# Performance work log

Measured on AMD Instinct MI355X. Metric: run time of the kernel, lower is better.

The kernel has to match this reference:

```python
import jax, jax.numpy as jnp
import numpy as np

H = 4        # nhead
TEMP = 0.1   # temperature
TOP_K = 5
SHAPE_EPS = 1e-5


def _ln(x, g, b):
    m = x.mean(-1, keepdims=True)
    v = ((x - m) ** 2).mean(-1, keepdims=True)
    return (x - m) / jnp.sqrt(v + SHAPE_EPS) * g + b


def _mha(x, Wqkv, bqkv, Wo, bo):
    B, L, D = x.shape
    Dh = D // H
    qkv = x @ Wqkv.T + bqkv                     # [B,L,3D]
    q, k, v = jnp.split(qkv, 3, axis=-1)
    q = q.reshape(B, L, H, Dh)
    k = k.reshape(B, L, H, Dh)
    v = v.reshape(B, L, H, Dh)
    att = jnp.einsum('bqhd,bkhd->bhqk', q, k) * (1.0 / np.sqrt(Dh))
    att = jax.nn.softmax(att, axis=-1)
    o = jnp.einsum('bhqk,bkhd->bqhd', att, v).reshape(B, L, D)
    return o @ Wo.T + bo


def _pattern_encoder(x, cls_token, Wqkv, bqkv, Wo, bo, ln1_g, ln1_b,
                     W1, b1, W2, b2, ln2_g, ln2_b, proj_W, proj_b, proj_g, proj_bb):
    B, L, D = x.shape
    h = jnp.concatenate([jnp.broadcast_to(cls_token, (B, 1, D)), x], axis=1)  # [B,L+1,D]
    for i in range(Wqkv.shape[0]):  # num_layers=2, post-norm (PyTorch default)
        a = _mha(h, Wqkv[i], bqkv[i], Wo[i], bo[i])
        h = _ln(h + a, ln1_g[i], ln1_b[i])
        f = jax.nn.gelu(h @ W1[i].T + b1[i], approximate=False) @ W2[i].T + b2[i]
        h = _ln(h + f, ln2_g[i], ln2_b[i])
    cls_out = h[:, 0, :]
    return _ln(cls_out @ proj_W.T + proj_b, proj_g, proj_bb)  # [B,d_repr]


def _value_encoder(xm, vW1, vb1, v_g, v_b, vW2, vb2):
    hh = _ln(xm @ vW1.T + vb1, v_g, v_b)
    return jax.nn.gelu(hh, approximate=False) @ vW2.T + vb2


def setup_inputs() -> dict:
    B, L, D, DR, N, P, NL = 64, 512, 512, 128, 10000, 96, 2
    key = jax.random.key(0)
    ks = jax.random.split(key, 16)
    sc = 0.02
    inp = {
        'query': jax.random.normal(ks[0], (B, L, D), jnp.float32),
        'memory_keys': jax.random.normal(ks[1], (N, DR), jnp.float32),
        'memory_values': jax.random.normal(ks[2], (N, P, D), jnp.float32),
        'cls_token': jax.random.normal(ks[3], (1, 1, D), jnp.float32) * sc,
        'Wqkv': jax.random.normal(ks[4], (NL, 3 * D, D), jnp.float32) * sc,
        'bqkv': jnp.zeros((NL, 3 * D), jnp.float32),
        'Wo': jax.random.normal(ks[5], (NL, D, D), jnp.float32) * sc,
        'bo': jnp.zeros((NL, D), jnp.float32),
        'ln1_g': jnp.ones((NL, D), jnp.float32),
        'ln1_b': jnp.zeros((NL, D), jnp.float32),
        'W1': jax.random.normal(ks[6], (NL, 2 * D, D), jnp.float32) * sc,
        'b1': jnp.zeros((NL, 2 * D), jnp.float32),
        'W2': jax.random.normal(ks[7], (NL, D, 2 * D), jnp.float32) * sc,
        'b2': jnp.zeros((NL, D), jnp.float32),
        'ln2_g': jnp.ones((NL, D), jnp.float32),
        'ln2_b': jnp.zeros((NL, D), jnp.float32),
        'proj_W': jax.random.normal(ks[8], (DR, D), jnp.float32) * sc,
        'proj_b': jnp.zeros((DR,), jnp.float32),
        'proj_g': jnp.ones((DR,), jnp.float32),
        'proj_bb': jnp.zeros((DR,), jnp.float32),
        'vW1': jax.random.normal(ks[9], (DR, D), jnp.float32) * sc,
        'vb1': jnp.zeros((DR,), jnp.float32),
        'v_g': jnp.ones((DR,), jnp.float32),
        'v_b': jnp.zeros((DR,), jnp.float32),
        'vW2': jax.random.normal(ks[10], (DR, DR), jnp.float32) * sc,
        'vb2': jnp.zeros((DR,), jnp.float32),
        'shape_w': jnp.float32(0.5),
    }
    return inp


def reference(query, memory_keys, memory_values, cls_token, Wqkv, bqkv, Wo, bo,
              ln1_g, ln1_b, W1, b1, W2, b2, ln2_g, ln2_b,
              proj_W, proj_b, proj_g, proj_bb, vW1, vb1, v_g, v_b, vW2, vb2, shape_w):
    q_repr = _pattern_encoder(query, cls_token, Wqkv, bqkv, Wo, bo, ln1_g, ln1_b,
                              W1, b1, W2, b2, ln2_g, ln2_b, proj_W, proj_b, proj_g, proj_bb)
    q_val = _value_encoder(query.mean(axis=1), vW1, vb1, v_g, v_b, vW2, vb2)
    qk = shape_w * q_repr + (1.0 - shape_w) * q_val              # [B,DR]
    # squared euclidean distance, expanded form (same math as sum((a-b)^2))
    d = ((qk ** 2).sum(-1)[:, None]
         - 2.0 * qk @ memory_keys.T
         + (memory_keys ** 2).sum(-1)[None, :])                  # [B,N]
    sim = -d / TEMP
    top_scores, top_idx = jax.lax.top_k(sim, TOP_K)              # [B,K]
    weights = jax.nn.softmax(top_scores, axis=-1)
    retrieved = memory_values[top_idx]                           # [B,K,P,D]
    return retrieved, weights
```

## Files before the change

kernel.cpp:

```cpp
#include <hip/hip_runtime.h>
#include <math.h>

#define B_    64
#define LQ    512
#define LC    513
#define DD    512
#define HH    4
#define DH    128
#define DRr   128
#define NKEYS 10000
#define PP    96
#define TOPK  5
#define MROWS (B_*LC)
#define VTSTRIDE 544

typedef __attribute__((ext_vector_type(8))) short short8v;
typedef __attribute__((ext_vector_type(4))) float f32x4;

static __device__ __forceinline__ float gelu_exact(float x) {
    return 0.5f * x * (1.0f + erff(x * 0.70710678118654752440f));
}

static __device__ __forceinline__ unsigned short f2bf(float x) {
    union { float f; unsigned u; } v; v.f = x;
    unsigned r = v.u + 0x7fff + ((v.u >> 16) & 1);
    return (unsigned short)(r >> 16);
}
static __device__ __forceinline__ float bf2f(unsigned short h) {
    union { float f; unsigned u; } v; v.u = ((unsigned)h) << 16;
    return v.f;
}
static __device__ __forceinline__ void split_bf(float x, unsigned short& hi, unsigned short& lo) {
    hi = f2bf(x);
    lo = f2bf(x - bf2f(hi));
}

__global__ __launch_bounds__(256)
void split_kernel(const float* __restrict__ x, unsigned short* __restrict__ hi,
                  unsigned short* __restrict__ lo, int n4)
{
    int i = blockIdx.x * blockDim.x + threadIdx.x;
    if (i >= n4) return;
    float4 v = ((const float4*)x)[i];
    unsigned short h0,h1,h2,h3,l0,l1,l2,l3;
    split_bf(v.x,h0,l0); split_bf(v.y,h1,l1); split_bf(v.z,h2,l2); split_bf(v.w,h3,l3);
    ((uint2*)hi)[i] = make_uint2((unsigned)h0 | ((unsigned)h1 << 16), (unsigned)h2 | ((unsigned)h3 << 16));
    ((uint2*)lo)[i] = make_uint2((unsigned)l0 | ((unsigned)l1 << 16), (unsigned)l2 | ((unsigned)l3 << 16));
}

__global__ __launch_bounds__(128)
void concat_cls(const float* __restrict__ query, const float* __restrict__ cls,
                float* __restrict__ h, unsigned short* __restrict__ h_hi,
                unsigned short* __restrict__ h_lo)
{
    int row = blockIdx.x;
    int t = threadIdx.x;
    int b = row / LC, r = row - b * LC;
    const float* src = (r == 0) ? cls : (query + ((size_t)b * LQ + (r - 1)) * DD);
    float4 v = *(const float4*)(src + t * 4);
    *(float4*)(h + (size_t)row * DD + t * 4) = v;
    unsigned short hs[4], ls[4];
    split_bf(v.x, hs[0], ls[0]); split_bf(v.y, hs[1], ls[1]);
    split_bf(v.z, hs[2], ls[2]); split_bf(v.w, hs[3], ls[3]);
    size_t o = (size_t)row * DD + t * 4;
    ((uint2*)(h_hi))[o >> 2] = make_uint2((unsigned)hs[0] | ((unsigned)hs[1]<<16),
                                          (unsigned)hs[2] | ((unsigned)hs[3]<<16));
    ((uint2*)(h_lo))[o >> 2] = make_uint2((unsigned)ls[0] | ((unsigned)ls[1]<<16),
                                          (unsigned)ls[2] | ((unsigned)ls[3]<<16));
}

#define BM 128
#define BN 128
#define BK 32
#define LDST 40

#define MFMA16(a, b, c) __builtin_amdgcn_mfma_f32_16x16x32_bf16(a, b, c, 0, 0, 0)

template<int MODE>
__global__ __launch_bounds__(256)
void gemm3(const unsigned short* __restrict__ Ahi, const unsigned short* __restrict__ Alo,
           const unsigned short* __restrict__ Whi, const unsigned short* __restrict__ Wlo,
           const float* __restrict__ bias, const float* __restrict__ res,
           float* __restrict__ Cf, unsigned short* __restrict__ Chi,
           unsigned short* __restrict__ Clo, unsigned short* __restrict__ Vhi,
           unsigned short* __restrict__ Vlo, int M, int N, int K)
{
    __shared__ __align__(16) unsigned short Ah[BM][LDST];
    __shared__ __align__(16) unsigned short Al[BM][LDST];
    __shared__ __align__(16) unsigned short Bh[BN][LDST];
    __shared__ __align__(16) unsigned short Bl[BN][LDST];

    const int t = threadIdx.x;
    const int lane = t & 63, w = t >> 6;
    const int wr = w >> 1, wc = w & 1;
    const int row0 = blockIdx.x * BM, col0 = blockIdx.y * BN;

    const int sr = t >> 1;
    const int sc = (t & 1) * 16;
    int agr = row0 + sr; if (agr >= M) agr = M - 1;
    const size_t aoff = (size_t)agr * K + sc;
    const size_t boff = (size_t)(col0 + sr) * K + sc;

    f32x4 acc[4][4];
    #pragma unroll
    for (int m = 0; m < 4; m++)
        #pragma unroll
        for (int n = 0; n < 4; n++) { acc[m][n][0]=0.f; acc[m][n][1]=0.f; acc[m][n][2]=0.f; acc[m][n][3]=0.f; }

    const int fr = lane & 15;
    const int fk = (lane >> 4) * 8;

    short8v sa_h[2], sa_l[2], sb_h[2], sb_l[2];
    {
        const short8v* p;
        p = (const short8v*)(Ahi + aoff); sa_h[0] = p[0]; sa_h[1] = p[1];
        p = (const short8v*)(Alo + aoff); sa_l[0] = p[0]; sa_l[1] = p[1];
        p = (const short8v*)(Whi + boff); sb_h[0] = p[0]; sb_h[1] = p[1];
        p = (const short8v*)(Wlo + boff); sb_l[0] = p[0]; sb_l[1] = p[1];
    }

    const int KT = K / BK;
    for (int kt = 0; kt < KT; kt++) {
        __syncthreads();
        *(short8v*)&Ah[sr][sc] = sa_h[0]; *(short8v*)&Ah[sr][sc + 8] = sa_h[1];
        *(short8v*)&Al[sr][sc] = sa_l[0]; *(short8v*)&Al[sr][sc + 8] = sa_l[1];
        *(short8v*)&Bh[sr][sc] = sb_h[0]; *(short8v*)&Bh[sr][sc + 8] = sb_h[1];
        *(short8v*)&Bl[sr][sc] = sb_l[0]; *(short8v*)&Bl[sr][sc + 8] = sb_l[1];
        __syncthreads();

        short8v ah[4], al[4], bh[4], bl[4];
        #pragma unroll
        for (int m = 0; m < 4; m++) {
            int r = wr * 64 + m * 16 + fr;
            ah[m] = *(const short8v*)&Ah[r][fk];
            al[m] = *(const short8v*)&Al[r][fk];
        }
        #pragma unroll
        for (int n = 0; n < 4; n++) {
            int c = wc * 64 + n * 16 + fr;
            bh[n] = *(const short8v*)&Bh[c][fk];
            bl[n] = *(const short8v*)&Bl[c][fk];
        }

        if (kt + 1 < KT) {
            int k0n = (kt + 1) * BK;
            const short8v* p;
            p = (const short8v*)(Ahi + aoff + k0n); sa_h[0] = p[0]; sa_h[1] = p[1];
            p = (const short8v*)(Alo + aoff + k0n); sa_l[0] = p[0]; sa_l[1] = p[1];
            p = (const short8v*)(Whi + boff + k0n); sb_h[0] = p[0]; sb_h[1] = p[1];
            p = (const short8v*)(Wlo + boff + k0n); sb_l[0] = p[0]; sb_l[1] = p[1];
        }

        #pragma unroll
        for (int m = 0; m < 4; m++)
            #pragma unroll
            for (int n = 0; n < 4; n++) {
                acc[m][n] = MFMA16(ah[m], bh[n], acc[m][n]);
                acc[m][n] = MFMA16(al[m], bh[n], acc[m][n]);
                acc[m][n] = MFMA16(ah[m], bl[n], acc[m][n]);
            }
    }

    #pragma unroll
    for (int m = 0; m < 4; m++) {
        int rb = row0 + wr * 64 + m * 16 + (lane >> 4) * 4;
        #pragma unroll
        for (int n = 0; n < 4; n++) {
            int c = col0 + wc * 64 + n * 16 + fr;
            float bcol = bias[c];
            #pragma unroll
            for (int r = 0; r < 4; r++) {
                int row = rb + r;
                if (row < M) {
                    float v = acc[m][n][r] + bcol;
                    if (MODE == 1) v += res[(size_t)row * N + c];
                    if (MODE == 2) {
                        v = gelu_exact(v);
                        unsigned short hv, lv;
                        split_bf(v, hv, lv);
                        Chi[(size_t)row * N + c] = hv;
                        Clo[(size_t)row * N + c] = lv;
                    } else if (MODE == 3) {
                        unsigned short hv, lv;
                        split_bf(v, hv, lv);
                        if (c < 1024) {
                            Chi[(size_t)row * 1024 + c] = hv;
                            Clo[(size_t)row * 1024 + c] = lv;
                        } else {
                            int da = c - 1024, hh = da >> 7, dd = da & 127;
                            int bb = row / LC, ll = row - bb * LC;
                            size_t vi = ((size_t)((bb * HH + hh) * DH + dd)) * VTSTRIDE + ll;
                            Vhi[vi] = hv; Vlo[vi] = lv;
                        }
                    } else {
                        Cf[(size_t)row * N + c] = v;
                    }
                }
            }
        }
    }
}

#define AQT 64
#define AKT 32
#define NKT2 17
__global__ __launch_bounds__(256)
void attn_mfma(const unsigned short* __restrict__ qkhi, const unsigned short* __restrict__ qklo,
               const unsigned short* __restrict__ vthi, const unsigned short* __restrict__ vtlo,
               unsigned short* __restrict__ ohi, unsigned short* __restrict__ olo)
{
    __shared__ __align__(16) unsigned short SM[24064];
    #define KH(r,d) SM[(r)*136 + (d)]
    #define KL(r,d) SM[4352 + (r)*136 + (d)]
    #define VH(d,k) SM[8704 + (d)*40 + (k)]
    #define VL(d,k) SM[13824 + (d)*40 + (k)]
    #define PH(r,k) SM[18944 + (r)*40 + (k)]
    #define PL(r,k) SM[21504 + (r)*40 + (k)]
    #define OS(r,d) SM[(r)*136 + (d)]

    const int t = threadIdx.x;
    const int lane = t & 63, w = t >> 6;
    const int qt = blockIdx.x, h = blockIdx.y, b = blockIdx.z;
    const int q0 = qt * AQT;
    const int c = lane & 15, g = lane >> 4;
    const float SCALE = 0.08838834764831845f;

    short8v qh[4], ql[4];
    {
        int qrow = b * LC + q0 + w * 16 + c;
        if (qrow > MROWS - 1) qrow = MROWS - 1;
        const unsigned short* bh_ = qkhi + (size_t)qrow * 1024 + h * DH;
        const unsigned short* bl_ = qklo + (size_t)qrow * 1024 + h * DH;
        #pragma unroll
        for (int ks = 0; ks < 4; ks++) {
            qh[ks] = *(const short8v*)(bh_ + ks * 32 + g * 8);
            ql[ks] = *(const short8v*)(bl_ + ks * 32 + g * 8);
        }
    }

    float m_r[4], l_r[4];
    #pragma unroll
    for (int r = 0; r < 4; r++) { m_r[r] = -INFINITY; l_r[r] = 0.f; }
    f32x4 acc_o[8];
    #pragma unroll
    for (int n = 0; n < 8; n++) { acc_o[n][0]=0.f; acc_o[n][1]=0.f; acc_o[n][2]=0.f; acc_o[n][3]=0.f; }

    const int skr = t >> 3, skd = (t & 7) * 16;
    const int svd = t >> 1, svk = (t & 1) * 16;

    for (int kt = 0; kt < NKT2; kt++) {
        __syncthreads();
        {
            int krow = b * LC + kt * AKT + skr;
            if (krow > MROWS - 1) krow = MROWS - 1;
            const unsigned short* kb  = qkhi + (size_t)krow * 1024 + 512 + h * DH + skd;
            const unsigned short* kbl = qklo + (size_t)krow * 1024 + 512 + h * DH + skd;
            *(short8v*)&KH(skr, skd)     = *(const short8v*)kb;
            *(short8v*)&KH(skr, skd + 8) = *(const short8v*)(kb + 8);
            *(short8v*)&KL(skr, skd)     = *(const short8v*)kbl;
            *(short8v*)&KL(skr, skd + 8) = *(const short8v*)(kbl + 8);
            const unsigned short* vb  = vthi + ((size_t)((b * HH + h) * DH + svd)) * VTSTRIDE + kt * AKT + svk;
            const unsigned short* vbl = vtlo + ((size_t)((b * HH + h) * DH + svd)) * VTSTRIDE + kt * AKT + svk;
            *(short8v*)&VH(svd, svk)     = *(const short8v*)vb;
            *(short8v*)&VH(svd, svk + 8) = *(const short8v*)(vb + 8);
            *(short8v*)&VL(svd, svk)     = *(const short8v*)vbl;
            *(short8v*)&VL(svd, svk + 8) = *(const short8v*)(vbl + 8);
        }
        __syncthreads();

        f32x4 s[2];
        s[0][0]=s[0][1]=s[0][2]=s[0][3]=0.f;
        s[1][0]=s[1][1]=s[1][2]=s[1][3]=0.f;
        #pragma unroll
        for (int n = 0; n < 2; n++) {
            #pragma unroll
            for (int ks = 0; ks < 4; ks++) {
                short8v kh = *(const short8v*)&KH(n * 16 + c, ks * 32 + g * 8);
                short8v kl = *(const short8v*)&KL(n * 16 + c, ks * 32 + g * 8);
                s[n] = MFMA16(qh[ks], kh, s[n]);
                s[n] = MFMA16(ql[ks], kh, s[n]);
                s[n] = MFMA16(qh[ks], kl, s[n]);
            }
        }

        #pragma unroll
        for (int n = 0; n < 2; n++) {
            bool oob = (kt * 32 + n * 16 + c) >= LC;
            #pragma unroll
            for (int r = 0; r < 4; r++) {
                float sv = s[n][r] * SCALE;
                s[n][r] = oob ? -INFINITY : sv;
            }
        }

        float alpha[4], p0v[4], p1v[4];
        #pragma unroll
        for (int r = 0; r < 4; r++) {
            float rm = fmaxf(s[0][r], s[1][r]);
            #pragma unroll
            for (int off = 1; off < 16; off <<= 1) rm = fmaxf(rm, __shfl_xor(rm, off));
            float mn = fmaxf(m_r[r], rm);
            float p0 = expf(s[0][r] - mn);
            float p1 = expf(s[1][r] - mn);
            float ts = p0 + p1;
            #pragma unroll
            for (int off = 1; off < 16; off <<= 1) ts += __shfl_xor(ts, off);
            float al = expf(m_r[r] - mn);
            m_r[r] = mn;
            l_r[r] = al * l_r[r] + ts;
            alpha[r] = al;
            p0v[r] = p0; p1v[r] = p1;
        }

        #pragma unroll
        for (int n = 0; n < 8; n++)
            #pragma unroll
            for (int r = 0; r < 4; r++) acc_o[n][r] *= alpha[r];

        #pragma unroll
        for (int r = 0; r < 4; r++) {
            unsigned short ph, pl;
            split_bf(p0v[r], ph, pl);
            PH(w * 16 + g * 4 + r, c) = ph;
            PL(w * 16 + g * 4 + r, c) = pl;
            split_bf(p1v[r], ph, pl);
            PH(w * 16 + g * 4 + r, 16 + c) = ph;
            PL(w * 16 + g * 4 + r, 16 + c) = pl;
        }
        __syncthreads();

        short8v pah = *(const short8v*)&PH(w * 16 + c, g * 8);
        short8v pal = *(const short8v*)&PL(w * 16 + c, g * 8);
        #pragma unroll
        for (int n = 0; n < 8; n++) {
            short8v vh = *(const short8v*)&VH(n * 16 + c, g * 8);
            short8v vl = *(const short8v*)&VL(n * 16 + c, g * 8);
            acc_o[n] = MFMA16(pah, vh, acc_o[n]);
            acc_o[n] = MFMA16(pal, vh, acc_o[n]);
            acc_o[n] = MFMA16(pah, vl, acc_o[n]);
        }
    }

    float inv[4];
    #pragma unroll
    for (int r = 0; r < 4; r++) inv[r] = 1.0f / l_r[r];

    const int orow = t >> 2, oc0 = (t & 3) * 32;
    #pragma unroll
    for (int pass = 0; pass < 2; pass++) {
        __syncthreads();
        #pragma unroll
        for (int n = 0; n < 8; n++)
            #pragma unroll
            for (int r = 0; r < 4; r++) {
                float v = acc_o[n][r] * inv[r];
                unsigned short hv, lv;
                split_bf(v, hv, lv);
                OS(w * 16 + g * 4 + r, n * 16 + c) = pass ? lv : hv;
            }
        __syncthreads();
        int grow = q0 + orow;
        if (grow < LC) {
            unsigned short* dst = (pass ? olo : ohi) + ((size_t)(b * LC + grow)) * DD + h * DH + oc0;
            #pragma unroll
            for (int u = 0; u < 4; u++)
                *(short8v*)(dst + u * 8) = *(const short8v*)&OS(orow, oc0 + u * 8);
        }
    }
    #undef KH
    #undef KL
    #undef VH
    #undef VL
    #undef PH
    #undef PL
    #undef OS
}

__global__ __launch_bounds__(128)
void ln512(const float* __restrict__ X, const float* __restrict__ g,
           const float* __restrict__ bb, float* __restrict__ Y,
           unsigned short* __restrict__ Yhi, unsigned short* __restrict__ Ylo)
{
    __shared__ float red[2];
    int row = blockIdx.x, t = threadIdx.x;
    const float* x = X + (size_t)row * DD;
    float4 v = *(const float4*)(x + t * 4);
    float s = v.x + v.y + v.z + v.w;
    #pragma unroll
    for (int off = 1; off < 64; off <<= 1) s += __shfl_xor(s, off);
    if ((t & 63) == 0) red[t >> 6] = s;
    __syncthreads();
    float mean = (red[0] + red[1]) * (1.0f / 512.0f);
    __syncthreads();
    float d0 = v.x - mean, d1 = v.y - mean, d2 = v.z - mean, d3 = v.w - mean;
    float s2 = d0 * d0 + d1 * d1 + d2 * d2 + d3 * d3;
    #pragma unroll
    for (int off = 1; off < 64; off <<= 1) s2 += __shfl_xor(s2, off);
    if ((t & 63) == 0) red[t >> 6] = s2;
    __syncthreads();
    float var = (red[0] + red[1]) * (1.0f / 512.0f);
    float rstd = 1.0f / sqrtf(var + 1e-5f);
    float4 gv = *(const float4*)(g + t * 4);
    float4 bv = *(const float4*)(bb + t * 4);
    float4 ov;
    ov.x = d0 * rstd * gv.x + bv.x;
    ov.y = d1 * rstd * gv.y + bv.y;
    ov.z = d2 * rstd * gv.z + bv.z;
    ov.w = d3 * rstd * gv.w + bv.w;
    size_t o = (size_t)row * DD + t * 4;
    *(float4*)(Y + o) = ov;
    unsigned short hs[4], ls[4];
    split_bf(ov.x, hs[0], ls[0]); split_bf(ov.y, hs[1], ls[1]);
    split_bf(ov.z, hs[2], ls[2]); split_bf(ov.w, hs[3], ls[3]);
    ((uint2*)Yhi)[o >> 2] = make_uint2((unsigned)hs[0] | ((unsigned)hs[1]<<16),
                                       (unsigned)hs[2] | ((unsigned)hs[3]<<16));
    ((uint2*)Ylo)[o >> 2] = make_uint2((unsigned)ls[0] | ((unsigned)ls[1]<<16),
                                       (unsigned)ls[2] | ((unsigned)ls[3]<<16));
}

__global__ __launch_bounds__(128)
void mean_l(const float* __restrict__ query, float* __restrict__ xm)
{
    int b = blockIdx.x, t = threadIdx.x;
    const float* base = query + (size_t)b * LQ * DD + t * 4;
    float ax = 0.f, ay = 0.f, az = 0.f, aw = 0.f;
    for (int l = 0; l < LQ; l++) {
        float4 v = *(const float4*)(base + (size_t)l * DD);
        ax += v.x; ay += v.y; az += v.z; aw += v.w;
    }
    float4 o = make_float4(ax * (1.f/512.f), ay * (1.f/512.f), az * (1.f/512.f), aw * (1.f/512.f));
    *(float4*)(xm + (size_t)b * DD + t * 4) = o;
}

static __device__ __forceinline__ float block128_sum(float x, float* red, int t) {
    #pragma unroll
    for (int off = 1; off < 64; off <<= 1) x += __shfl_xor(x, off);
    if ((t & 63) == 0) red[t >> 6] = x;
    __syncthreads();
    float r = red[0] + red[1];
    __syncthreads();
    return r;
}

__global__ __launch_bounds__(128)
void proj_ln(const float* __restrict__ h, const float* __restrict__ pW, const float* __restrict__ pb,
             const float* __restrict__ pg, const float* __restrict__ pbb, float* __restrict__ q_repr)
{
    __shared__ float xs[DD];
    __shared__ float red[2];
    int b = blockIdx.x, t = threadIdx.x;
    *(float4*)&xs[t * 4] = *(const float4*)(h + (size_t)(b * LC) * DD + t * 4);
    __syncthreads();
    const float* w = pW + (size_t)t * DD;
    float acc = pb[t];
    for (int k = 0; k < DD; k += 4) {
        float4 a = *(const float4*)&xs[k];
        float4 ww = *(const float4*)(w + k);
        acc += a.x * ww.x + a.y * ww.y + a.z * ww.z + a.w * ww.w;
    }
    float mean = block128_sum(acc, red, t) * (1.f / 128.f);
    float dx = acc - mean;
    float var = block128_sum(dx * dx, red, t) * (1.f / 128.f);
    float rstd = 1.0f / sqrtf(var + 1e-5f);
    q_repr[(size_t)b * DRr + t] = dx * rstd * pg[t] + pbb[t];
}

__global__ __launch_bounds__(128)
void venc(const float* __restrict__ xm, const float* __restrict__ vW1, const float* __restrict__ vb1,
          const float* __restrict__ vg, const float* __restrict__ vb,
          const float* __restrict__ vW2, const float* __restrict__ vb2,
          float* __restrict__ q_val)
{
    __shared__ float xs[DD];
    __shared__ float hg[DRr];
    __shared__ float red[2];
    int b = blockIdx.x, t = threadIdx.x;
    *(float4*)&xs[t * 4] = *(const float4*)(xm + (size_t)b * DD + t * 4);
    __syncthreads();
    const float* w = vW1 + (size_t)t * DD;
    float acc = vb1[t];
    for (int k = 0; k < DD; k += 4) {
        float4 a = *(const float4*)&xs[k];
        float4 ww = *(const float4*)(w + k);
        acc += a.x * ww.x + a.y * ww.y + a.z * ww.z + a.w * ww.w;
    }
    float mean = block128_sum(acc, red, t) * (1.f / 128.f);
    float dx = acc - mean;
    float var = block128_sum(dx * dx, red, t) * (1.f / 128.f);
    float rstd = 1.0f / sqrtf(var + 1e-5f);
    float hn = dx * rstd * vg[t] + vb[t];
    hg[t] = gelu_exact(hn);
    __syncthreads();
    const float* w2 = vW2 + (size_t)t * DRr;
    float acc2 = vb2[t];
    for (int k = 0; k < DRr; k += 4) {
        float4 a = *(const float4*)&hg[k];
        float4 ww = *(const float4*)(w2 + k);
        acc2 += a.x * ww.x + a.y * ww.y + a.z * ww.z + a.w * ww.w;
    }
    q_val[(size_t)b * DRr + t] = acc2;
}

__global__ void combine_qk(const float* __restrict__ qr, const float* __restrict__ qv,
                           const float* __restrict__ swp, float* __restrict__ qk)
{
    int i = blockIdx.x * blockDim.x + threadIdx.x;
    if (i < B_ * DRr) {
        float sw = swp[0];
        qk[i] = sw * qr[i] + (1.f - sw) * qv[i];
    }
}

__global__ __launch_bounds__(256)
void sim_kernel(const float* __restrict__ qk, const float* __restrict__ mkeys, float* __restrict__ sim)
{
    __shared__ float qs[DRr];
    int b = blockIdx.x, t = threadIdx.x;
    if (t < DRr) qs[t] = qk[(size_t)b * DRr + t];
    __syncthreads();
    float qn = 0.f;
    #pragma unroll 8
    for (int i = 0; i < DRr; i++) qn += qs[i] * qs[i];
    for (int n = t; n < NKEYS; n += 256) {
        const float* kr = mkeys + (size_t)n * DRr;
        float dot = 0.f, kn = 0.f;
        #pragma unroll 8
        for (int i = 0; i < DRr; i += 4) {
            float4 kv = *(const float4*)(kr + i);
            dot += qs[i] * kv.x + qs[i + 1] * kv.y + qs[i + 2] * kv.z + qs[i + 3] * kv.w;
            kn  += kv.x * kv.x + kv.y * kv.y + kv.z * kv.z + kv.w * kv.w;
        }
        float d = qn - 2.f * dot + kn;
        sim[(size_t)b * NKEYS + n] = -d / 0.1f;
    }
}

static __device__ __forceinline__ void topk_insert(float* v, int* id, float x, int n) {
    bool better = (x > v[TOPK - 1]) || (x == v[TOPK - 1] && n < id[TOPK - 1]);
    if (better) {
        v[TOPK - 1] = x; id[TOPK - 1] = n;
        #pragma unroll
        for (int k = TOPK - 1; k > 0; k--) {
            bool sw = (v[k] > v[k - 1]) || (v[k] == v[k - 1] && id[k] < id[k - 1]);
            if (!sw) break;
            float tv = v[k]; v[k] = v[k - 1]; v[k - 1] = tv;
            int ti = id[k]; id[k] = id[k - 1]; id[k - 1] = ti;
        }
    }
}

__global__ __launch_bounds__(256)
void topk_kernel(const float* __restrict__ sim, int* __restrict__ topidx, float* __restrict__ wout)
{
    __shared__ float sv[256][TOPK];
    __shared__ int   si[256][TOPK];
    int b = blockIdx.x, t = threadIdx.x;
    float v[TOPK]; int id[TOPK];
    #pragma unroll
    for (int k = 0; k < TOPK; k++) { v[k] = -INFINITY; id[k] = 0x7fffffff; }
    for (int n = t; n < NKEYS; n += 256) {
        topk_insert(v, id, sim[(size_t)b * NKEYS + n], n);
    }
    #pragma unroll
    for (int k = 0; k < TOPK; k++) { sv[t][k] = v[k]; si[t][k] = id[k]; }
    for (int strd = 128; strd >= 1; strd >>= 1) {
        __syncthreads();
        if (t < strd) {
            #pragma unroll
            for (int k = 0; k < TOPK; k++) topk_insert(v, id, sv[t + strd][k], si[t + strd][k]);
            #pragma unroll
            for (int k = 0; k < TOPK; k++) { sv[t][k] = v[k]; si[t][k] = id[k]; }
        }
    }
    if (t == 0) {
        float m = v[0];
        float e[TOPK]; float sum = 0.f;
        #pragma unroll
        for (int k = 0; k < TOPK; k++) { e[k] = expf(v[k] - m); sum += e[k]; }
        #pragma unroll
        for (int k = 0; k < TOPK; k++) {
            wout[(size_t)b * TOPK + k] = e[k] / sum;
            topidx[b * TOPK + k] = id[k];
        }
    }
}

__global__ __launch_bounds__(128)
void gather_kernel(const float* __restrict__ mv, const int* __restrict__ topidx, float* __restrict__ out)
{
    int blk = blockIdx.x;
    int b = blk / (TOPK * PP);
    int rem = blk - b * (TOPK * PP);
    int k = rem / PP;
    int p = rem - k * PP;
    int idx = topidx[b * TOPK + k];
    const float4* src = (const float4*)(mv + ((size_t)idx * PP + p) * DD);
    float4* dst = (float4*)(out + (size_t)blk * DD);
    dst[threadIdx.x] = src[threadIdx.x];
}

extern "C" void kernel_launch(void* const* d_in, const int* in_sizes, int n_in,
                              void* d_out, int out_size, void* d_ws, size_t ws_size,
                              hipStream_t stream) {
    const float* query = (const float*)d_in[0];
    const float* mkeys = (const float*)d_in[1];
    const float* mvals = (const float*)d_in[2];
    const float* cls   = (const float*)d_in[3];
    const float* Wqkv  = (const float*)d_in[4];
    const float* bqkv  = (const float*)d_in[5];
    const float* Wo    = (const float*)d_in[6];
    const float* bo    = (const float*)d_in[7];
    const float* ln1g  = (const float*)d_in[8];
    const float* ln1b  = (const float*)d_in[9];
    const float* W1    = (const float*)d_in[10];
    const float* b1    = (const float*)d_in[11];
    const float* W2    = (const float*)d_in[12];
    const float* b2    = (const float*)d_in[13];
    const float* ln2g  = (const float*)d_in[14];
    const float* ln2b  = (const float*)d_in[15];
    const float* pW    = (const float*)d_in[16];
    const float* pb    = (const float*)d_in[17];
    const float* pg    = (const float*)d_in[18];
    const float* pbb   = (const float*)d_in[19];
    const float* vW1   = (const float*)d_in[20];
    const float* vb1   = (const float*)d_in[21];
    const float* vg    = (const float*)d_in[22];
    const float* vb    = (const float*)d_in[23];
    const float* vW2   = (const float*)d_in[24];
    const float* vb2   = (const float*)d_in[25];
    const float* swp   = (const float*)d_in[26];
    float* out = (float*)d_out;

    float* ws    = (float*)d_ws;
    float* h     = ws;
    float* preln = h + (size_t)MROWS * DD;
    unsigned short* h_hi  = (unsigned short*)(preln + (size_t)MROWS * DD);
    unsigned short* h_lo  = h_hi  + (size_t)MROWS * DD;
    unsigned short* mid_hi = h_lo + (size_t)MROWS * DD;
    unsigned short* mid_lo = mid_hi + (size_t)MROWS * 1024;
    unsigned short* qkhi  = mid_lo + (size_t)MROWS * 1024;
    unsigned short* qklo  = qkhi  + (size_t)MROWS * 1024;
    unsigned short* vthi  = qklo  + (size_t)MROWS * 1024;
    unsigned short* vtlo  = vthi  + (size_t)32768 * VTSTRIDE;
    unsigned short* wq_hi = vtlo  + (size_t)32768 * VTSTRIDE;
    unsigned short* wq_lo = wq_hi + (size_t)2 * 1536 * DD;
    unsigned short* wo_hi = wq_lo + (size_t)2 * 1536 * DD;
    unsigned short* wo_lo = wo_hi + (size_t)2 * DD * DD;
    unsigned short* w1_hi = wo_lo + (size_t)2 * DD * DD;
    unsigned short* w1_lo = w1_hi + (size_t)2 * 1024 * DD;
    unsigned short* w2_hi = w1_lo + (size_t)2 * 1024 * DD;
    unsigned short* w2_lo = w2_hi + (size_t)2 * DD * 1024;
    float* xm   = (float*)(w2_lo + (size_t)2 * DD * 1024);
    float* qval = xm   + (size_t)B_ * DD;
    float* qrep = qval + (size_t)B_ * DRr;
    float* qkc  = qrep + (size_t)B_ * DRr;
    float* simb = qkc  + (size_t)B_ * DRr;
    int*   tidx = (int*)(simb + (size_t)B_ * NKEYS);
    (void)ws_size; (void)in_sizes; (void)n_in; (void)out_size;

    {
        int n4;
        n4 = 2 * 1536 * DD / 4;
        split_kernel<<<(n4 + 255) / 256, 256, 0, stream>>>(Wqkv, wq_hi, wq_lo, n4);
        n4 = 2 * DD * DD / 4;
        split_kernel<<<(n4 + 255) / 256, 256, 0, stream>>>(Wo, wo_hi, wo_lo, n4);
        n4 = 2 * 1024 * DD / 4;
        split_kernel<<<(n4 + 255) / 256, 256, 0, stream>>>(W1, w1_hi, w1_lo, n4);
        n4 = 2 * DD * 1024 / 4;
        split_kernel<<<(n4 + 255) / 256, 256, 0, stream>>>(W2, w2_hi, w2_lo, n4);
    }

    concat_cls<<<MROWS, 128, 0, stream>>>(query, cls, h, h_hi, h_lo);

    for (int l = 0; l < 2; l++) {
        const unsigned short* wqh = wq_hi + (size_t)l * 1536 * DD;
        const unsigned short* wql = wq_lo + (size_t)l * 1536 * DD;
        const unsigned short* woh = wo_hi + (size_t)l * DD * DD;
        const unsigned short* wol = wo_lo + (size_t)l * DD * DD;
        const unsigned short* w1h = w1_hi + (size_t)l * 1024 * DD;
        const unsigned short* w1l = w1_lo + (size_t)l * 1024 * DD;
        const unsigned short* w2h = w2_hi + (size_t)l * DD * 1024;
        const unsigned short* w2l = w2_lo + (size_t)l * DD * 1024;
        const float* bq  = bqkv + (size_t)l * 1536;
        const float* bol = bo   + (size_t)l * DD;
        const float* g1  = ln1g + (size_t)l * DD;
        const float* be1 = ln1b + (size_t)l * DD;
        const float* b1l = b1   + (size_t)l * 1024;
        const float* b2l = b2   + (size_t)l * DD;
        const float* g2  = ln2g + (size_t)l * DD;
        const float* be2 = ln2b + (size_t)l * DD;

        gemm3<3><<<dim3(257, 12), 256, 0, stream>>>(h_hi, h_lo, wqh, wql, bq, nullptr,
                                                    nullptr, qkhi, qklo, vthi, vtlo,
                                                    MROWS, 1536, DD);
        attn_mfma<<<dim3(9, HH, B_), 256, 0, stream>>>(qkhi, qklo, vthi, vtlo, h_hi, h_lo);
        gemm3<1><<<dim3(257, 4), 256, 0, stream>>>(h_hi, h_lo, woh, wol, bol, h,
                                                   preln, nullptr, nullptr, nullptr, nullptr,
                                                   MROWS, DD, DD);
        ln512<<<MROWS, 128, 0, stream>>>(preln, g1, be1, h, h_hi, h_lo);
        gemm3<2><<<dim3(257, 8), 256, 0, stream>>>(h_hi, h_lo, w1h, w1l, b1l, nullptr,
                                                   nullptr, mid_hi, mid_lo, nullptr, nullptr,
                                                   MROWS, 1024, DD);
        gemm3<1><<<dim3(257, 4), 256, 0, stream>>>(mid_hi, mid_lo, w2h, w2l, b2l, h,
                                                   preln, nullptr, nullptr, nullptr, nullptr,
                                                   MROWS, DD, 1024);
        ln512<<<MROWS, 128, 0, stream>>>(preln, g2, be2, h, h_hi, h_lo);
    }

    proj_ln<<<B_, 128, 0, stream>>>(h, pW, pb, pg, pbb, qrep);
    mean_l<<<B_, 128, 0, stream>>>(query, xm);
    venc<<<B_, 128, 0, stream>>>(xm, vW1, vb1, vg, vb, vW2, vb2, qval);
    combine_qk<<<(B_ * DRr + 255) / 256, 256, 0, stream>>>(qrep, qval, swp, qkc);
    sim_kernel<<<B_, 256, 0, stream>>>(qkc, mkeys, simb);
    topk_kernel<<<B_, 256, 0, stream>>>(simb, tidx, out + (size_t)B_ * TOPK * PP * DD);
    gather_kernel<<<B_ * TOPK * PP, 128, 0, stream>>>(mvals, tidx, out);
}
```

Before: 2.833 ms.

## Use direct global-to-LDS loads with XOR swizzle in GEMM; split mean and sim kernels

```diff
diff --git a/kernel.cpp b/kernel.cpp
--- a/kernel.cpp
+++ b/kernel.cpp
@@ -33,6 +33,12 @@
 static __device__ __forceinline__ void split_bf(float x, unsigned short& hi, unsigned short& lo) {
     hi = f2bf(x);
     lo = f2bf(x - bf2f(hi));
+}
+
+static __device__ __forceinline__ void gload16(const unsigned short* g, unsigned short* l) {
+    __builtin_amdgcn_global_load_lds(
+        (const __attribute__((address_space(1))) unsigned*)g,
+        (__attribute__((address_space(3))) unsigned*)l, 16, 0, 0);
 }
 
 __global__ __launch_bounds__(256)
@@ -72,7 +78,6 @@
 #define BM 128
 #define BN 128
 #define BK 32
-#define LDST 40
 
 #define MFMA16(a, b, c) __builtin_amdgcn_mfma_f32_16x16x32_bf16(a, b, c, 0, 0, 0)
 
@@ -85,21 +90,27 @@
            unsigned short* __restrict__ Clo, unsigned short* __restrict__ Vhi,
            unsigned short* __restrict__ Vlo, int M, int N, int K)
 {
-    __shared__ __align__(16) unsigned short Ah[BM][LDST];
-    __shared__ __align__(16) unsigned short Al[BM][LDST];
-    __shared__ __align__(16) unsigned short Bh[BN][LDST];
-    __shared__ __align__(16) unsigned short Bl[BN][LDST];
+    __shared__ __align__(16) unsigned short LAh[4096];
+    __shared__ __align__(16) unsigned short LAl[4096];
+    __shared__ __align__(16) unsigned short LBh[4096];
+    __shared__ __align__(16) unsigned short LBl[4096];
 
     const int t = threadIdx.x;
     const int lane = t & 63, w = t >> 6;
     const int wr = w >> 1, wc = w & 1;
     const int row0 = blockIdx.x * BM, col0 = blockIdx.y * BN;
 
-    const int sr = t >> 1;
-    const int sc = (t & 1) * 16;
-    int agr = row0 + sr; if (agr >= M) agr = M - 1;
-    const size_t aoff = (size_t)agr * K + sc;
-    const size_t boff = (size_t)(col0 + sr) * K + sc;
+    const int srow = t >> 2;
+    const int sg   = t & 3;
+    const int glog = sg ^ ((srow >> 1) & 3);
+    int ar0 = row0 + srow;      if (ar0 >= M) ar0 = M - 1;
+    int ar1 = row0 + srow + 64; if (ar1 >= M) ar1 = M - 1;
+    const size_t aoff0 = (size_t)ar0 * K + glog * 8;
+    const size_t aoff1 = (size_t)ar1 * K + glog * 8;
+    const size_t boff0 = (size_t)(col0 + srow) * K + glog * 8;
+    const size_t boff1 = (size_t)(col0 + srow + 64) * K + glog * 8;
+    const int ldso0 = t * 8;
+    const int ldso1 = t * 8 + 2048;
 
     f32x4 acc[4][4];
     #pragma unroll
@@ -107,48 +118,36 @@
         #pragma unroll
         for (int n = 0; n < 4; n++) { acc[m][n][0]=0.f; acc[m][n][1]=0.f; acc[m][n][2]=0.f; acc[m][n][3]=0.f; }
 
-    const int fr = lane & 15;
-    const int fk = (lane >> 4) * 8;
-
-    short8v sa_h[2], sa_l[2], sb_h[2], sb_l[2];
-    {
-        const short8v* p;
-        p = (const short8v*)(Ahi + aoff); sa_h[0] = p[0]; sa_h[1] = p[1];
-        p = (const short8v*)(Alo + aoff); sa_l[0] = p[0]; sa_l[1] = p[1];
-        p = (const short8v*)(Whi + boff); sb_h[0] = p[0]; sb_h[1] = p[1];
-        p = (const short8v*)(Wlo + boff); sb_l[0] = p[0]; sb_l[1] = p[1];
-    }
+    const int c = lane & 15;
+    const int g = lane >> 4;
+    const int gs = (g ^ ((c >> 1) & 3)) * 8;
 
     const int KT = K / BK;
     for (int kt = 0; kt < KT; kt++) {
+        const int k0 = kt * BK;
         __syncthreads();
-        *(short8v*)&Ah[sr][sc] = sa_h[0]; *(short8v*)&Ah[sr][sc + 8] = sa_h[1];
-        *(short8v*)&Al[sr][sc] = sa_l[0]; *(short8v*)&Al[sr][sc + 8] = sa_l[1];
-        *(short8v*)&Bh[sr][sc] = sb_h[0]; *(short8v*)&Bh[sr][sc + 8] = sb_h[1];
-        *(short8v*)&Bl[sr][sc] = sb_l[0]; *(short8v*)&Bl[sr][sc + 8] = sb_l[1];
+        gload16(Ahi + aoff0 + k0, &LAh[ldso0]);
+        gload16(Ahi + aoff1 + k0, &LAh[ldso1]);
+        gload16(Alo + aoff0 + k0, &LAl[ldso0]);
+        gload16(Alo + aoff1 + k0, &LAl[ldso1]);
+        gload16(Whi + boff0 + k0, &LBh[ldso0]);
+        gload16(Whi + boff1 + k0, &LBh[ldso1]);
+        gload16(Wlo + boff0 + k0, &LBl[ldso0]);
+        gload16(Wlo + boff1 + k0, &LBl[ldso1]);
         __syncthreads();
 
         short8v ah[4], al[4], bh[4], bl[4];
         #pragma unroll
         for (int m = 0; m < 4; m++) {
-            int r = wr * 64 + m * 16 + fr;
-            ah[m] = *(const short8v*)&Ah[r][fk];
-            al[m] = *(const short8v*)&Al[r][fk];
+            int off = (wr * 64 + m * 16 + c) * 32 + gs;
+            ah[m] = *(const short8v*)&LAh[off];
+            al[m] = *(const short8v*)&LAl[off];
         }
         #pragma unroll
         for (int n = 0; n < 4; n++) {
-            int c = wc * 64 + n * 16 + fr;
-            bh[n] = *(const short8v*)&Bh[c][fk];
-            bl[n] = *(const short8v*)&Bl[c][fk];
-        }
-
-        if (kt + 1 < KT) {
-            int k0n = (kt + 1) * BK;
-            const short8v* p;
-            p = (const short8v*)(Ahi + aoff + k0n); sa_h[0] = p[0]; sa_h[1] = p[1];
-            p = (const short8v*)(Alo + aoff + k0n); sa_l[0] = p[0]; sa_l[1] = p[1];
-            p = (const short8v*)(Whi + boff + k0n); sb_h[0] = p[0]; sb_h[1] = p[1];
-            p = (const short8v*)(Wlo + boff + k0n); sb_l[0] = p[0]; sb_l[1] = p[1];
+            int off = (wc * 64 + n * 16 + c) * 32 + gs;
+            bh[n] = *(const short8v*)&LBh[off];
+            bl[n] = *(const short8v*)&LBl[off];
         }
 
         #pragma unroll
@@ -166,34 +165,34 @@
         int rb = row0 + wr * 64 + m * 16 + (lane >> 4) * 4;
         #pragma unroll
         for (int n = 0; n < 4; n++) {
-            int c = col0 + wc * 64 + n * 16 + fr;
-            float bcol = bias[c];
+            int cc = col0 + wc * 64 + n * 16 + c;
+            float bcol = bias[cc];
             #pragma unroll
             for (int r = 0; r < 4; r++) {
                 int row = rb + r;
                 if (row < M) {
                     float v = acc[m][n][r] + bcol;
-                    if (MODE == 1) v += res[(size_t)row * N + c];
+                    if (MODE == 1) v += res[(size_t)row * N + cc];
                     if (MODE == 2) {
                         v = gelu_exact(v);
                         unsigned short hv, lv;
                         split_bf(v, hv, lv);
-                        Chi[(size_t)row * N + c] = hv;
-                        Clo[(size_t)row * N + c] = lv;
+                        Chi[(size_t)row * N + cc] = hv;
+                        Clo[(size_t)row * N + cc] = lv;
                     } else if (MODE == 3) {
                         unsigned short hv, lv;
                         split_bf(v, hv, lv);
-                        if (c < 1024) {
-                            Chi[(size_t)row * 1024 + c] = hv;
-                            Clo[(size_t)row * 1024 + c] = lv;
+                        if (cc < 1024) {
+                            Chi[(size_t)row * 1024 + cc] = hv;
+                            Clo[(size_t)row * 1024 + cc] = lv;
                         } else {
-                            int da = c - 1024, hh = da >> 7, dd = da & 127;
+                            int da = cc - 1024, hh = da >> 7, dd = da & 127;
                             int bb = row / LC, ll = row - bb * LC;
                             size_t vi = ((size_t)((bb * HH + hh) * DH + dd)) * VTSTRIDE + ll;
                             Vhi[vi] = hv; Vlo[vi] = lv;
                         }
                     } else {
-                        Cf[(size_t)row * N + c] = v;
+                        Cf[(size_t)row * N + cc] = v;
                     }
                 }
             }
@@ -419,17 +418,30 @@
 }
 
 __global__ __launch_bounds__(128)
-void mean_l(const float* __restrict__ query, float* __restrict__ xm)
-{
-    int b = blockIdx.x, t = threadIdx.x;
-    const float* base = query + (size_t)b * LQ * DD + t * 4;
+void mean_part(const float* __restrict__ query, float* __restrict__ part)
+{
+    int b = blockIdx.x, ch = blockIdx.y, t = threadIdx.x;
+    const float* base = query + ((size_t)b * LQ + ch * 64) * DD + t * 4;
     float ax = 0.f, ay = 0.f, az = 0.f, aw = 0.f;
-    for (int l = 0; l < LQ; l++) {
+    for (int l = 0; l < 64; l++) {
         float4 v = *(const float4*)(base + (size_t)l * DD);
         ax += v.x; ay += v.y; az += v.z; aw += v.w;
     }
-    float4 o = make_float4(ax * (1.f/512.f), ay * (1.f/512.f), az * (1.f/512.f), aw * (1.f/512.f));
-    *(float4*)(xm + (size_t)b * DD + t * 4) = o;
+    *(float4*)(part + ((size_t)(b * 8 + ch)) * DD + t * 4) = make_float4(ax, ay, az, aw);
+}
+
+__global__ __launch_bounds__(128)
+void mean_fin(const float* __restrict__ part, float* __restrict__ xm)
+{
+    int b = blockIdx.x, t = threadIdx.x;
+    float ax = 0.f, ay = 0.f, az = 0.f, aw = 0.f;
+    #pragma unroll
+    for (int ch = 0; ch < 8; ch++) {
+        float4 v = *(const float4*)(part + ((size_t)(b * 8 + ch)) * DD + t * 4);
+        ax += v.x; ay += v.y; az += v.z; aw += v.w;
+    }
+    *(float4*)(xm + (size_t)b * DD + t * 4) =
+        make_float4(ax * (1.f/512.f), ay * (1.f/512.f), az * (1.f/512.f), aw * (1.f/512.f));
 }
 
 static __device__ __forceinline__ float block128_sum(float x, float* red, int t) {
@@ -511,17 +523,19 @@
     }
 }
 
+#define SIMCH 10
 __global__ __launch_bounds__(256)
 void sim_kernel(const float* __restrict__ qk, const float* __restrict__ mkeys, float* __restrict__ sim)
 {
     __shared__ float qs[DRr];
-    int b = blockIdx.x, t = threadIdx.x;
+    int b = blockIdx.x, ch = blockIdx.y, t = threadIdx.x;
     if (t < DRr) qs[t] = qk[(size_t)b * DRr + t];
     __syncthreads();
     float qn = 0.f;
     #pragma unroll 8
     for (int i = 0; i < DRr; i++) qn += qs[i] * qs[i];
-    for (int n = t; n < NKEYS; n += 256) {
+    int n0 = ch * (NKEYS / SIMCH), n1 = n0 + (NKEYS / SIMCH);
+    for (int n = n0 + t; n < n1; n += 256) {
         const float* kr = mkeys + (size_t)n * DRr;
         float dot = 0.f, kn = 0.f;
         #pragma unroll 8
@@ -656,6 +670,7 @@
     float* qkc  = qrep + (size_t)B_ * DRr;
     float* simb = qkc  + (size_t)B_ * DRr;
     int*   tidx = (int*)(simb + (size_t)B_ * NKEYS);
+    float* mpart = (float*)(tidx + 512);
     (void)ws_size; (void)in_sizes; (void)n_in; (void)out_size;
 
     {
@@ -708,10 +723,11 @@
     }
 
     proj_ln<<<B_, 128, 0, stream>>>(h, pW, pb, pg, pbb, qrep);
-    mean_l<<<B_, 128, 0, stream>>>(query, xm);
+    mean_part<<<dim3(B_, 8), 128, 0, stream>>>(query, mpart);
+    mean_fin<<<B_, 128, 0, stream>>>(mpart, xm);
     venc<<<B_, 128, 0, stream>>>(xm, vW1, vb1, vg, vb, vW2, vb2, qval);
     combine_qk<<<(B_ * DRr + 255) / 256, 256, 0, stream>>>(qrep, qval, swp, qkc);
-    sim_kernel<<<B_, 256, 0, stream>>>(qkc, mkeys, simb);
+    sim_kernel<<<dim3(B_, SIMCH), 256, 0, stream>>>(qkc, mkeys, simb);
     topk_kernel<<<B_, 256, 0, stream>>>(simb, tidx, out + (size_t)B_ * TOPK * PP * DD);
     gather_kernel<<<B_ * TOPK * PP, 128, 0, stream>>>(mvals, tidx, out);
 }
```

After: 2.499 ms. -11.8%, faster.
